# Optimization experiments

Hardware: AMD Instinct MI355X
Metric: run time of the kernel (lower is better)

## Reference

```python
import jax, jax.numpy as jnp
import numpy as np

ALPHA = 0.2  # LeakyReLU negative slope
NEG_INF = -9e15


def setup_inputs() -> dict:
    key = jax.random.key(0)
    k1, k2, k3, k4 = jax.random.split(key, 4)
    B, N, F_in, F_out = 8, 2048, 256, 128
    x = jax.random.normal(k1, (B, N, F_in), dtype=jnp.float32)
    adj = jax.random.randint(k2, (B, N, N), 0, 2, dtype=jnp.int32)
    # xavier-uniform-like init
    limW = float(np.sqrt(6.0 / (F_in + F_out)))
    W = jax.random.uniform(k3, (F_in, F_out), jnp.float32, -limW, limW)
    lima = float(np.sqrt(6.0 / (2 * F_out + 1)))
    a = jax.random.uniform(k4, (2 * F_out, 1), jnp.float32, -lima, lima)
    return {"x": x, "adj": adj, "W": W, "a": a}


def reference(x, adj, W, a):
    # x: [B, N, F_in], adj: [B, N, N], W: [F_in, F_out], a: [2*F_out, 1]
    F_out = W.shape[1]
    h = jnp.einsum('bnf,fo->bno', x, W)            # [B, N, F_out]
    a1 = a[:F_out, 0]                               # attends to source node i
    a2 = a[F_out:, 0]                               # attends to target node j
    f1 = h @ a1                                     # [B, N]
    f2 = h @ a2                                     # [B, N]
    # e[b,i,j] = leakyrelu(a1.h_i + a2.h_j) -- factored form of the concat trick
    e = jax.nn.leaky_relu(f1[:, :, None] + f2[:, None, :], negative_slope=ALPHA)
    attention = jnp.where(adj > 0, e, NEG_INF)
    attention = jax.nn.softmax(attention, axis=2)   # [B, N, N]
    # dropout is identity in eval mode
    h_prime = jnp.einsum('bij,bjo->bio', attention, h)  # [B, N, F_out]
    return jax.nn.elu(h_prime)                      # concat=True -> ELU
```

## Files before the change

kernel.cpp:

```cpp
#include <hip/hip_runtime.h>
#include <stdint.h>

#define BB   8
#define NN   2048
#define FIN  256
#define FOUT 128

using short8 = __attribute__((ext_vector_type(8))) short;
using f32x4  = __attribute__((ext_vector_type(4))) float;

__device__ __forceinline__ unsigned short rbf(float f) {
    return (unsigned short)((__float_as_uint(f) + 0x8000u) >> 16);
}

__device__ __forceinline__ void mfma_calib(int m, int quad, int* Mlab, int* Nlab) {
    short8 pa1, pb1, pa2, pb2;
    const short one = (short)0x3F80;
    const short mb  = (short)rbf((float)m);
#pragma unroll
    for (int j = 0; j < 8; ++j) { pa1[j] = 0; pa2[j] = 0; pb1[j] = mb; pb2[j] = one; }
    if (quad == 0) { pa1[0] = one; pa2[0] = mb; }
    f32x4 zz = {0.f, 0.f, 0.f, 0.f};
    f32x4 c1 = __builtin_amdgcn_mfma_f32_16x16x32_bf16(pa1, pb1, zz, 0, 0, 0);
    f32x4 c2 = __builtin_amdgcn_mfma_f32_16x16x32_bf16(pa2, pb2, zz, 0, 0, 0);
#pragma unroll
    for (int r = 0; r < 4; ++r) {
        Nlab[r] = ((int)c1[r]) & 15;
        Mlab[r] = ((int)c2[r]) & 15;
    }
}

__global__ __launch_bounds__(256) void gat_wt(const float* __restrict__ W,
                                              unsigned short* __restrict__ wt) {
    const int g  = blockIdx.x * 256 + threadIdx.x;
    const int k  = g >> 5;
    const int o4 = (g & 31) << 2;
    float4 wv = *(const float4*)(W + (k << 7) + o4);
    wt[((o4 + 0) << 8) + k] = rbf(wv.x);
    wt[((o4 + 1) << 8) + k] = rbf(wv.y);
    wt[((o4 + 2) << 8) + k] = rbf(wv.z);
    wt[((o4 + 3) << 8) + k] = rbf(wv.w);
}

__global__ __launch_bounds__(256) void gat_h2(
        const float* __restrict__ x, const unsigned short* __restrict__ wt,
        const float* __restrict__ a, unsigned short* __restrict__ ht,
        float* __restrict__ f1, float* __restrict__ f2) {
    __shared__ float hs[64][129];
    const int tid  = threadIdx.x;
    const int w    = tid >> 6;
    const int lane = tid & 63;
    const int m    = lane & 15;
    const int quad = lane >> 4;
    const int R0   = blockIdx.x << 6;
    const int gi   = R0 + (w << 4) + m;

    int Mlab[4], Nlab[4];
    mfma_calib(m, quad, Mlab, Nlab);

    f32x4 zz = {0.f, 0.f, 0.f, 0.f};
    f32x4 acc[8];
#pragma unroll
    for (int t = 0; t < 8; ++t) acc[t] = zz;

    const float* xrow = x + (size_t)gi * FIN;
#pragma unroll
    for (int kc = 0; kc < 8; ++kc) {
        const int k0 = (kc << 5) + (quad << 3);
        float4 xa = *(const float4*)(xrow + k0);
        float4 xb = *(const float4*)(xrow + k0 + 4);
        short8 av;
        av[0] = (short)rbf(xa.x); av[1] = (short)rbf(xa.y);
        av[2] = (short)rbf(xa.z); av[3] = (short)rbf(xa.w);
        av[4] = (short)rbf(xb.x); av[5] = (short)rbf(xb.y);
        av[6] = (short)rbf(xb.z); av[7] = (short)rbf(xb.w);
#pragma unroll
        for (int ot = 0; ot < 8; ++ot) {
            short8 bw = *(const short8*)(wt + ((((ot << 4) + m) << 8) + k0));
            acc[ot] = __builtin_amdgcn_mfma_f32_16x16x32_bf16(av, bw, acc[ot], 0, 0, 0);
        }
    }

#pragma unroll
    for (int ot = 0; ot < 8; ++ot)
#pragma unroll
        for (int r = 0; r < 4; ++r)
            hs[(w << 4) + Mlab[r]][(ot << 4) + Nlab[r]] = acc[ot][r];
    __syncthreads();

    {
        const int i  = tid >> 2;
        const int ch = (tid & 3) << 5;
        float s1 = 0.f, s2 = 0.f;
#pragma unroll
        for (int u = 0; u < 32; ++u) {
            float hv = hs[i][ch + u];
            s1 = fmaf(hv, a[ch + u], s1);
            s2 = fmaf(hv, a[FOUT + ch + u], s2);
        }
        s1 += __shfl_xor(s1, 1); s1 += __shfl_xor(s1, 2);
        s2 += __shfl_xor(s2, 1); s2 += __shfl_xor(s2, 2);
        if ((tid & 3) == 0) { f1[R0 + i] = s1; f2[R0 + i] = s2; }
    }

    {
        const int b   = R0 >> 11;
        const int il0 = R0 & (NN - 1);
#pragma unroll
        for (int v = 0; v < 4; ++v) {
            const int u   = (v << 8) + tid;
            const int o   = u >> 3;
            const int io8 = (u & 7) << 3;
            short8 hv;
#pragma unroll
            for (int e = 0; e < 8; ++e) hv[e] = (short)rbf(hs[io8 + e][o]);
            *(short8*)(ht + ((size_t)((b << 7) + o) << 11) + il0 + io8) = hv;
        }
    }
}

__global__ __launch_bounds__(256, 4) void gat_s2(
        const int* __restrict__ adj, const unsigned short* __restrict__ ht,
        const float* __restrict__ f1, const float* __restrict__ f2,
        float* __restrict__ out) {
    const int bk   = blockIdx.x;
    const int b    = bk & 7;
    const int i0   = (bk >> 3) << 4;
    const int tid  = threadIdx.x;
    const int w    = tid >> 6;
    const int lane = tid & 63;
    const int m    = lane & 15;
    const int quad = lane >> 4;

    __shared__ float sbuf[4][16];
    __shared__ float accbuf[4][16][128];

    int Mlab[4], Nlab[4];
    mfma_calib(m, quad, Mlab, Nlab);

    const float f1r = f1[(b << 11) + i0 + m];
    const int*  adjrow = adj + ((size_t)((b << 11) + i0 + m) << 11);
    const float* f2b = f2 + (b << 11);
    const unsigned short* htb = ht + ((size_t)b << 18);

    f32x4 zz = {0.f, 0.f, 0.f, 0.f};
    f32x4 acc[8];
#pragma unroll
    for (int t2 = 0; t2 < 8; ++t2) acc[t2] = zz;
    float ssum = 0.f;

    const int jb = (w << 9) + (quad << 3);
    int4   aj0 = *(const int4*)(adjrow + jb);
    int4   aj1 = *(const int4*)(adjrow + jb + 4);
    float4 fa  = *(const float4*)(f2b + jb);
    float4 fb  = *(const float4*)(f2b + jb + 4);

#pragma unroll
    for (int c = 0; c < 16; ++c) {
        const int j0 = jb + (c << 5);
        short8 hf[8];
#pragma unroll
        for (int ot = 0; ot < 8; ++ot)
            hf[ot] = *(const short8*)(htb + ((((ot << 4) + m) << 11) + j0));

        int4 na0, na1; float4 nf0, nf1;
        if (c < 15) {
            na0 = *(const int4*)(adjrow + j0 + 32);
            na1 = *(const int4*)(adjrow + j0 + 36);
            nf0 = *(const float4*)(f2b + j0 + 32);
            nf1 = *(const float4*)(f2b + j0 + 36);
        }

        float p[8];
        {
            float t0 = f1r + fa.x, t1 = f1r + fa.y, t2 = f1r + fa.z, t3 = f1r + fa.w;
            float t4 = f1r + fb.x, t5 = f1r + fb.y, t6 = f1r + fb.z, t7 = f1r + fb.w;
            p[0] = (aj0.x > 0) ? __expf(fmaxf(t0, 0.2f * t0)) : 0.f;
            p[1] = (aj0.y > 0) ? __expf(fmaxf(t1, 0.2f * t1)) : 0.f;
            p[2] = (aj0.z > 0) ? __expf(fmaxf(t2, 0.2f * t2)) : 0.f;
            p[3] = (aj0.w > 0) ? __expf(fmaxf(t3, 0.2f * t3)) : 0.f;
            p[4] = (aj1.x > 0) ? __expf(fmaxf(t4, 0.2f * t4)) : 0.f;
            p[5] = (aj1.y > 0) ? __expf(fmaxf(t5, 0.2f * t5)) : 0.f;
            p[6] = (aj1.z > 0) ? __expf(fmaxf(t6, 0.2f * t6)) : 0.f;
            p[7] = (aj1.w > 0) ? __expf(fmaxf(t7, 0.2f * t7)) : 0.f;
        }
        ssum += ((p[0] + p[1]) + (p[2] + p[3])) + ((p[4] + p[5]) + (p[6] + p[7]));

        short8 pf;
        pf[0] = (short)rbf(p[0]); pf[1] = (short)rbf(p[1]);
        pf[2] = (short)rbf(p[2]); pf[3] = (short)rbf(p[3]);
        pf[4] = (short)rbf(p[4]); pf[5] = (short)rbf(p[5]);
        pf[6] = (short)rbf(p[6]); pf[7] = (short)rbf(p[7]);

#pragma unroll
        for (int ot = 0; ot < 8; ++ot)
            acc[ot] = __builtin_amdgcn_mfma_f32_16x16x32_bf16(pf, hf[ot], acc[ot], 0, 0, 0);

        if (c < 15) { aj0 = na0; aj1 = na1; fa = nf0; fb = nf1; }
    }

    ssum += __shfl_xor(ssum, 16);
    ssum += __shfl_xor(ssum, 32);
    if (lane < 16) sbuf[w][lane] = ssum;
#pragma unroll
    for (int ot = 0; ot < 8; ++ot)
#pragma unroll
        for (int r = 0; r < 4; ++r)
            accbuf[w][Mlab[r]][(ot << 4) + Nlab[r]] = acc[ot][r];
    __syncthreads();

    {
        const int row = tid >> 4;
        const int o0  = (tid & 15) << 3;
        float s = (sbuf[0][row] + sbuf[1][row]) + (sbuf[2][row] + sbuf[3][row]);
        float inv = 1.0f / s;
        float v[8];
#pragma unroll
        for (int d = 0; d < 8; ++d)
            v[d] = (accbuf[0][row][o0 + d] + accbuf[1][row][o0 + d]) +
                   (accbuf[2][row][o0 + d] + accbuf[3][row][o0 + d]);
        float4 r0, r1;
        float y;
        y = v[0] * inv; r0.x = y > 0.f ? y : expm1f(y);
        y = v[1] * inv; r0.y = y > 0.f ? y : expm1f(y);
        y = v[2] * inv; r0.z = y > 0.f ? y : expm1f(y);
        y = v[3] * inv; r0.w = y > 0.f ? y : expm1f(y);
        y = v[4] * inv; r1.x = y > 0.f ? y : expm1f(y);
        y = v[5] * inv; r1.y = y > 0.f ? y : expm1f(y);
        y = v[6] * inv; r1.z = y > 0.f ? y : expm1f(y);
        y = v[7] * inv; r1.w = y > 0.f ? y : expm1f(y);
        float* orow = out + (((size_t)(b << 11) + i0 + row) << 7) + o0;
        *(float4*)(orow)     = r0;
        *(float4*)(orow + 4) = r1;
    }
}

extern "C" void kernel_launch(void* const* d_in, const int* in_sizes, int n_in,
                              void* d_out, int out_size, void* d_ws, size_t ws_size,
                              hipStream_t stream) {
    const float* x   = nullptr;
    const int*   adj = nullptr;
    const float* W   = nullptr;
    const float* a   = nullptr;
    for (int i = 0; i < n_in; ++i) {
        const long s = in_sizes[i];
        if      (s == (long)BB * NN * NN)  adj = (const int*)d_in[i];
        else if (s == (long)BB * NN * FIN) x   = (const float*)d_in[i];
        else if (s == (long)FIN * FOUT)    W   = (const float*)d_in[i];
        else if (s == 2L * FOUT)           a   = (const float*)d_in[i];
    }
    if (!x)   x   = (const float*)d_in[0];
    if (!adj) adj = (const int*)d_in[1];
    if (!W)   W   = (const float*)d_in[2];
    if (!a)   a   = (const float*)d_in[3];
    float* out = (float*)d_out;

    unsigned short* wt = (unsigned short*)d_ws;
    unsigned short* ht = wt + 32768;
    float* f1 = (float*)(ht + (size_t)BB * NN * FOUT);
    float* f2 = f1 + BB * NN;

    hipLaunchKernelGGL(gat_wt, dim3(32),   dim3(256), 0, stream, W, wt);
    hipLaunchKernelGGL(gat_h2, dim3(256),  dim3(256), 0, stream, x, wt, a, ht, f1, f2);
    hipLaunchKernelGGL(gat_s2, dim3(1024), dim3(256), 0, stream, adj, ht, f1, f2, out);
}
```

Measured before the change: 281.5 us.

## Stage attention probabilities through double-buffered LDS with coalesced adjacency reads

The attention kernel now has each wave compute probabilities for 4 rows with fully coalesced 256-wide adjacency and f2 loads. It writes bf16 P tiles into double-buffered shared memory, and all waves then consume them to run MFMAs over j-splits. Previously each lane read 8-int strided segments of its own row. The h-projection kernel is also split into 1024 blocks of 16 rows, staging bf16 x in LDS so each wave computes two output tiles. This should improve DRAM coalescing on the 134MB adjacency read and raise parallelism in the projection, at the cost of extra block barriers and LDS traffic.

```diff
diff --git a/kernel.cpp b/kernel.cpp
--- a/kernel.cpp
+++ b/kernel.cpp
@@ -42,87 +42,90 @@
     wt[((o4 + 3) << 8) + k] = rbf(wv.w);
 }
 
-__global__ __launch_bounds__(256) void gat_h2(
+__global__ __launch_bounds__(256) void gat_h3(
         const float* __restrict__ x, const unsigned short* __restrict__ wt,
         const float* __restrict__ a, unsigned short* __restrict__ ht,
         float* __restrict__ f1, float* __restrict__ f2) {
-    __shared__ float hs[64][129];
+    __shared__ unsigned short xs[16][264];
+    __shared__ float hs[16][132];
+    const int bk   = blockIdx.x;
+    const int R0   = bk << 4;
+    const int b    = R0 >> 11;
+    const int il0  = R0 & (NN - 1);
     const int tid  = threadIdx.x;
     const int w    = tid >> 6;
     const int lane = tid & 63;
     const int m    = lane & 15;
     const int quad = lane >> 4;
-    const int R0   = blockIdx.x << 6;
-    const int gi   = R0 + (w << 4) + m;
-
+
+#pragma unroll
+    for (int rr = 0; rr < 4; ++rr) {
+        const int row = (w << 2) + rr;
+        float4 xv = *(const float4*)(x + (size_t)(R0 + row) * FIN + (lane << 2));
+        ushort4 c4;
+        c4.x = rbf(xv.x); c4.y = rbf(xv.y); c4.z = rbf(xv.z); c4.w = rbf(xv.w);
+        *(ushort4*)(&xs[row][lane << 2]) = c4;
+    }
     int Mlab[4], Nlab[4];
     mfma_calib(m, quad, Mlab, Nlab);
+    __syncthreads();
 
     f32x4 zz = {0.f, 0.f, 0.f, 0.f};
-    f32x4 acc[8];
-#pragma unroll
-    for (int t = 0; t < 8; ++t) acc[t] = zz;
-
-    const float* xrow = x + (size_t)gi * FIN;
+    f32x4 acc[2] = {zz, zz};
 #pragma unroll
     for (int kc = 0; kc < 8; ++kc) {
         const int k0 = (kc << 5) + (quad << 3);
-        float4 xa = *(const float4*)(xrow + k0);
-        float4 xb = *(const float4*)(xrow + k0 + 4);
-        short8 av;
-        av[0] = (short)rbf(xa.x); av[1] = (short)rbf(xa.y);
-        av[2] = (short)rbf(xa.z); av[3] = (short)rbf(xa.w);
-        av[4] = (short)rbf(xb.x); av[5] = (short)rbf(xb.y);
-        av[6] = (short)rbf(xb.z); av[7] = (short)rbf(xb.w);
-#pragma unroll
-        for (int ot = 0; ot < 8; ++ot) {
-            short8 bw = *(const short8*)(wt + ((((ot << 4) + m) << 8) + k0));
-            acc[ot] = __builtin_amdgcn_mfma_f32_16x16x32_bf16(av, bw, acc[ot], 0, 0, 0);
-        }
-    }
-
-#pragma unroll
-    for (int ot = 0; ot < 8; ++ot)
+        short8 av = *(const short8*)(&xs[m][k0]);
+#pragma unroll
+        for (int t = 0; t < 2; ++t) {
+            const int ot = (w << 1) + t;
+            short8 bw = *(const short8*)(wt + (((ot << 4) + m) << 8) + k0);
+            acc[t] = __builtin_amdgcn_mfma_f32_16x16x32_bf16(av, bw, acc[t], 0, 0, 0);
+        }
+    }
+#pragma unroll
+    for (int t = 0; t < 2; ++t)
 #pragma unroll
         for (int r = 0; r < 4; ++r)
-            hs[(w << 4) + Mlab[r]][(ot << 4) + Nlab[r]] = acc[ot][r];
+            hs[Mlab[r]][(((w << 1) + t) << 4) + Nlab[r]] = acc[t][r];
     __syncthreads();
 
     {
-        const int i  = tid >> 2;
-        const int ch = (tid & 3) << 5;
+        const int i   = tid >> 4;
+        const int seg = tid & 15;
+        const int o0  = seg << 3;
         float s1 = 0.f, s2 = 0.f;
 #pragma unroll
-        for (int u = 0; u < 32; ++u) {
-            float hv = hs[i][ch + u];
-            s1 = fmaf(hv, a[ch + u], s1);
-            s2 = fmaf(hv, a[FOUT + ch + u], s2);
+        for (int e = 0; e < 8; ++e) {
+            float hv = hs[i][o0 + e];
+            s1 = fmaf(hv, a[o0 + e], s1);
+            s2 = fmaf(hv, a[FOUT + o0 + e], s2);
         }
         s1 += __shfl_xor(s1, 1); s1 += __shfl_xor(s1, 2);
+        s1 += __shfl_xor(s1, 4); s1 += __shfl_xor(s1, 8);
         s2 += __shfl_xor(s2, 1); s2 += __shfl_xor(s2, 2);
-        if ((tid & 3) == 0) { f1[R0 + i] = s1; f2[R0 + i] = s2; }
-    }
-
+        s2 += __shfl_xor(s2, 4); s2 += __shfl_xor(s2, 8);
+        if (seg == 0) { f1[R0 + i] = s1; f2[R0 + i] = s2; }
+    }
     {
-        const int b   = R0 >> 11;
-        const int il0 = R0 & (NN - 1);
-#pragma unroll
-        for (int v = 0; v < 4; ++v) {
-            const int u   = (v << 8) + tid;
-            const int o   = u >> 3;
-            const int io8 = (u & 7) << 3;
-            short8 hv;
-#pragma unroll
-            for (int e = 0; e < 8; ++e) hv[e] = (short)rbf(hs[io8 + e][o]);
-            *(short8*)(ht + ((size_t)((b << 7) + o) << 11) + il0 + io8) = hv;
-        }
-    }
-}
-
-__global__ __launch_bounds__(256, 4) void gat_s2(
+        const int o  = tid >> 1;
+        const int i8 = (tid & 1) << 3;
+        short8 hv;
+#pragma unroll
+        for (int e = 0; e < 8; ++e) hv[e] = (short)rbf(hs[i8 + e][o]);
+        *(short8*)(ht + ((size_t)((b << 7) + o) << 11) + il0 + i8) = hv;
+    }
+}
+
+__global__ __launch_bounds__(256, 4) void gat_s3(
         const int* __restrict__ adj, const unsigned short* __restrict__ ht,
         const float* __restrict__ f1, const float* __restrict__ f2,
         float* __restrict__ out) {
+    alignas(16) __shared__ char smem[32832];
+    unsigned short* P = (unsigned short*)smem;
+    float (*accbuf)[16][128] = (float (*)[16][128])smem;
+    float* sred = (float*)(smem + 32768);
+
     const int bk   = blockIdx.x;
     const int b    = bk & 7;
     const int i0   = (bk >> 3) << 4;
@@ -132,76 +135,74 @@
     const int m    = lane & 15;
     const int quad = lane >> 4;
 
-    __shared__ float sbuf[4][16];
-    __shared__ float accbuf[4][16][128];
-
     int Mlab[4], Nlab[4];
     mfma_calib(m, quad, Mlab, Nlab);
 
-    const float f1r = f1[(b << 11) + i0 + m];
-    const int*  adjrow = adj + ((size_t)((b << 11) + i0 + m) << 11);
-    const float* f2b = f2 + (b << 11);
+    const int*   adjb = adj + ((size_t)((b << 11) + i0) << 11);
+    const float* f2b  = f2 + (b << 11);
     const unsigned short* htb = ht + ((size_t)b << 18);
+
+    float f1v[4];
+#pragma unroll
+    for (int rr = 0; rr < 4; ++rr) f1v[rr] = f1[(b << 11) + i0 + (w << 2) + rr];
 
     f32x4 zz = {0.f, 0.f, 0.f, 0.f};
     f32x4 acc[8];
 #pragma unroll
-    for (int t2 = 0; t2 < 8; ++t2) acc[t2] = zz;
-    float ssum = 0.f;
-
-    const int jb = (w << 9) + (quad << 3);
-    int4   aj0 = *(const int4*)(adjrow + jb);
-    int4   aj1 = *(const int4*)(adjrow + jb + 4);
-    float4 fa  = *(const float4*)(f2b + jb);
-    float4 fb  = *(const float4*)(f2b + jb + 4);
-
-#pragma unroll
-    for (int c = 0; c < 16; ++c) {
-        const int j0 = jb + (c << 5);
-        short8 hf[8];
-#pragma unroll
-        for (int ot = 0; ot < 8; ++ot)
-            hf[ot] = *(const short8*)(htb + ((((ot << 4) + m) << 11) + j0));
-
-        int4 na0, na1; float4 nf0, nf1;
-        if (c < 15) {
-            na0 = *(const int4*)(adjrow + j0 + 32);
-            na1 = *(const int4*)(adjrow + j0 + 36);
-            nf0 = *(const float4*)(f2b + j0 + 32);
-            nf1 = *(const float4*)(f2b + j0 + 36);
-        }
-
-        float p[8];
-        {
-            float t0 = f1r + fa.x, t1 = f1r + fa.y, t2 = f1r + fa.z, t3 = f1r + fa.w;
-            float t4 = f1r + fb.x, t5 = f1r + fb.y, t6 = f1r + fb.z, t7 = f1r + fb.w;
-            p[0] = (aj0.x > 0) ? __expf(fmaxf(t0, 0.2f * t0)) : 0.f;
-            p[1] = (aj0.y > 0) ? __expf(fmaxf(t1, 0.2f * t1)) : 0.f;
-            p[2] = (aj0.z > 0) ? __expf(fmaxf(t2, 0.2f * t2)) : 0.f;
-            p[3] = (aj0.w > 0) ? __expf(fmaxf(t3, 0.2f * t3)) : 0.f;
-            p[4] = (aj1.x > 0) ? __expf(fmaxf(t4, 0.2f * t4)) : 0.f;
-            p[5] = (aj1.y > 0) ? __expf(fmaxf(t5, 0.2f * t5)) : 0.f;
-            p[6] = (aj1.z > 0) ? __expf(fmaxf(t6, 0.2f * t6)) : 0.f;
-            p[7] = (aj1.w > 0) ? __expf(fmaxf(t7, 0.2f * t7)) : 0.f;
-        }
-        ssum += ((p[0] + p[1]) + (p[2] + p[3])) + ((p[4] + p[5]) + (p[6] + p[7]));
-
-        short8 pf;
-        pf[0] = (short)rbf(p[0]); pf[1] = (short)rbf(p[1]);
-        pf[2] = (short)rbf(p[2]); pf[3] = (short)rbf(p[3]);
-        pf[4] = (short)rbf(p[4]); pf[5] = (short)rbf(p[5]);
-        pf[6] = (short)rbf(p[6]); pf[7] = (short)rbf(p[7]);
-
-#pragma unroll
-        for (int ot = 0; ot < 8; ++ot)
-            acc[ot] = __builtin_amdgcn_mfma_f32_16x16x32_bf16(pf, hf[ot], acc[ot], 0, 0, 0);
-
-        if (c < 15) { aj0 = na0; aj1 = na1; fa = nf0; fb = nf1; }
-    }
-
-    ssum += __shfl_xor(ssum, 16);
-    ssum += __shfl_xor(ssum, 32);
-    if (lane < 16) sbuf[w][lane] = ssum;
+    for (int t = 0; t < 8; ++t) acc[t] = zz;
+    float sp[4] = {0.f, 0.f, 0.f, 0.f};
+
+    auto produce = [&](int C, int bb) {
+        float4 fj = *(const float4*)(f2b + C + (lane << 2));
+        float fv[4] = {fj.x, fj.y, fj.z, fj.w};
+#pragma unroll
+        for (int rr = 0; rr < 4; ++rr) {
+            const int row = (w << 2) + rr;
+            int4 av = *(const int4*)(adjb + ((size_t)row << 11) + C + (lane << 2));
+            int am[4] = {av.x, av.y, av.z, av.w};
+            const float f1r = f1v[rr];
+            ushort4 pk;
+            unsigned short* pkp = (unsigned short*)&pk;
+#pragma unroll
+            for (int u = 0; u < 4; ++u) {
+                float e = f1r + fv[u];
+                float p = (am[u] > 0) ? __expf(fmaxf(e, 0.2f * e)) : 0.f;
+                sp[rr] += p;
+                pkp[u] = rbf(p);
+            }
+            *(ushort4*)(P + bb * 4224 + row * 264 + (lane << 2)) = pk;
+        }
+    };
+    auto consume = [&](int C, int bb) {
+#pragma unroll
+        for (int t = 0; t < 2; ++t) {
+            const int jl = (((w << 1) + t) << 5) + (quad << 3);
+            short8 pa = *(const short8*)(P + bb * 4224 + m * 264 + jl);
+#pragma unroll
+            for (int ot = 0; ot < 8; ++ot) {
+                short8 hf = *(const short8*)(htb + ((size_t)((ot << 4) + m) << 11) + C + jl);
+                acc[ot] = __builtin_amdgcn_mfma_f32_16x16x32_bf16(pa, hf, acc[ot], 0, 0, 0);
+            }
+        }
+    };
+
+    produce(0, 0);
+#pragma unroll
+    for (int c = 0; c < 8; ++c) {
+        __syncthreads();
+        if (c < 7) produce((c + 1) << 8, (c + 1) & 1);
+        consume(c << 8, c & 1);
+    }
+    __syncthreads();
+
+#pragma unroll
+    for (int rr = 0; rr < 4; ++rr) {
+        float v = sp[rr];
+        v += __shfl_xor(v, 1);  v += __shfl_xor(v, 2);
+        v += __shfl_xor(v, 4);  v += __shfl_xor(v, 8);
+        v += __shfl_xor(v, 16); v += __shfl_xor(v, 32);
+        if (lane == 0) sred[(w << 2) + rr] = v;
+    }
 #pragma unroll
     for (int ot = 0; ot < 8; ++ot)
 #pragma unroll
@@ -212,8 +213,7 @@
     {
         const int row = tid >> 4;
         const int o0  = (tid & 15) << 3;
-        float s = (sbuf[0][row] + sbuf[1][row]) + (sbuf[2][row] + sbuf[3][row]);
-        float inv = 1.0f / s;
+        const float inv = 1.0f / sred[row];
         float v[8];
 #pragma unroll
         for (int d = 0; d < 8; ++d)
@@ -261,6 +261,6 @@
     float* f2 = f1 + BB * NN;
 
     hipLaunchKernelGGL(gat_wt, dim3(32),   dim3(256), 0, stream, W, wt);
-    hipLaunchKernelGGL(gat_h2, dim3(256),  dim3(256), 0, stream, x, wt, a, ht, f1, f2);
-    hipLaunchKernelGGL(gat_s2, dim3(1024), dim3(256), 0, stream, adj, ht, f1, f2, out);
-}
+    hipLaunchKernelGGL(gat_h3, dim3(1024), dim3(256), 0, stream, x, wt, a, ht, f1, f2);
+    hipLaunchKernelGGL(gat_s3, dim3(1024), dim3(256), 0, stream, adj, ht, f1, f2, out);
+}
```

Result: slower. 305.6 us (+8.5%).
